# Kernel optimization log

Measured on AMD Instinct MI355X. Metric: run time of the kernel, lower is better.

Reference implementation:

```python
import jax, jax.numpy as jnp
import numpy as np

D = 1024
H = 16
HD = D // H
T = 2048
B = 2
EPS = 1e-6


def rmsnorm(x, w):
    xf = x.astype(jnp.float32)
    n = xf * jax.lax.rsqrt(jnp.mean(xf * xf, axis=-1, keepdims=True) + EPS)
    return n.astype(x.dtype) * w


def setup_inputs() -> dict:
    key = jax.random.key(0)
    ks = jax.random.split(key, 12)
    s_in = 1.0 / np.sqrt(D)
    s_h = 1.0 / np.sqrt(HD * H)
    s_ff = 1.0 / np.sqrt(4 * D)
    return {
        "x": jax.random.normal(ks[0], (B, T, D), jnp.float32),
        "wq": jax.random.normal(ks[1], (H, D, HD), jnp.float32) * s_in,
        "wk": jax.random.normal(ks[2], (H, D, HD), jnp.float32) * s_in,
        "wv": jax.random.normal(ks[3], (H, D, HD), jnp.float32) * s_in,
        "w_proj": jax.random.normal(ks[4], (D, D), jnp.float32) * s_h,
        "b_proj": jax.random.normal(ks[5], (D,), jnp.float32) * 0.01,
        "w1": jax.random.normal(ks[6], (D, 8 * D), jnp.float32) * s_in,
        "b1": jax.random.normal(ks[7], (8 * D,), jnp.float32) * 0.01,
        "w2": jax.random.normal(ks[8], (4 * D, D), jnp.float32) * s_ff,
        "b2": jax.random.normal(ks[9], (D,), jnp.float32) * 0.01,
        "g1": jnp.ones((D,), jnp.float32),
        "g2": jnp.ones((D,), jnp.float32),
    }


def reference(x, wq, wk, wv, w_proj, b_proj, w1, b1, w2, b2, g1, g2):
    # --- attention sub-block ---
    xn = rmsnorm(x, g1)
    q = jnp.einsum("btd,hde->bhte", xn, wq)  # [B,H,T,HD]
    k = jnp.einsum("btd,hde->bhte", xn, wk)
    v = jnp.einsum("btd,hde->bhte", xn, wv)
    scores = jnp.einsum("bhte,bhse->bhts", q, k) * (HD ** -0.5)
    causal = jnp.tril(jnp.ones((T, T), bool))
    scores = jnp.where(causal, scores, -jnp.inf)
    attn = jax.nn.softmax(scores, axis=-1)
    o = jnp.einsum("bhts,bhse->bhte", attn, v)  # [B,H,T,HD]
    o = o.transpose(0, 2, 1, 3).reshape(B, T, H * HD)  # concat heads
    x = x + o @ w_proj + b_proj
    # --- GLU FFN sub-block ---
    xn2 = rmsnorm(x, g2)
    h = xn2 @ w1 + b1  # [B,T,8D]
    a, b = jnp.split(h, 2, axis=-1)
    glu = a * jax.nn.sigmoid(b)  # [B,T,4D]
    x = x + glu @ w2 + b2
    return x
```

## Files before the change

### kernel.cpp

```cpp
#include <hip/hip_runtime.h>


typedef __attribute__((ext_vector_type(4))) float f32x4;
typedef __attribute__((ext_vector_type(8))) short short8;

typedef __attribute__((address_space(1))) const void gvoid;
typedef __attribute__((address_space(3))) void lvoid;

static __device__ __forceinline__ void gl_lds16(const void* g, void* l) {
  __builtin_amdgcn_global_load_lds((gvoid*)g, (lvoid*)l, 16, 0, 0);
}

static __device__ __forceinline__ unsigned short f2bf(float f) {
  union { float f; unsigned u; } v; v.f = f;
  unsigned r = v.u + 0x7fffu + ((v.u >> 16) & 1u);
  return (unsigned short)(r >> 16);
}
static __device__ __forceinline__ float to_f32(float v) { return v; }
static __device__ __forceinline__ float to_f32(unsigned short v) {
  union { unsigned u; float f; } x; x.u = ((unsigned)v) << 16; return x.f;
}

static __device__ __forceinline__ f32x4 mfma16(short8 a, short8 b, f32x4 c) {
  return __builtin_amdgcn_mfma_f32_16x16x32_bf16(a, b, c, 0, 0, 0);
}

__global__ __launch_bounds__(256) void prep_all(
    const float* __restrict__ wq, const float* __restrict__ wk,
    const float* __restrict__ wv, const float* __restrict__ wproj,
    const float* __restrict__ w1, const float* __restrict__ w2,
    unsigned short* __restrict__ wt_qkv, unsigned short* __restrict__ wpt,
    unsigned short* __restrict__ w1t, unsigned short* __restrict__ w2t,
    const float* __restrict__ x, const float* __restrict__ g1,
    unsigned short* __restrict__ xn)
{
  __shared__ float tile[64][65];
  const int bid = blockIdx.x;
  if (bid >= 4096) {
    int row = bid - 4096;
    int t = threadIdx.x;
    float4 v = ((const float4*)(x + (long)row * 1024))[t];
    float ss = v.x * v.x + v.y * v.y + v.z * v.z + v.w * v.w;
#pragma unroll
    for (int ofs = 32; ofs; ofs >>= 1) ss += __shfl_down(ss, ofs);
    float* red = &tile[0][0];
    if ((t & 63) == 0) red[t >> 6] = ss;
    __syncthreads();
    float sc = rsqrtf((red[0] + red[1] + red[2] + red[3]) * (1.0f / 1024.0f) + 1e-6f);
    float4 gv = ((const float4*)g1)[t];
    ushort4 o4;
    o4.x = f2bf(v.x * sc * gv.x); o4.y = f2bf(v.y * sc * gv.y);
    o4.z = f2bf(v.z * sc * gv.z); o4.w = f2bf(v.w * sc * gv.w);
    ((ushort4*)(xn + (long)row * 1024))[t] = o4;
    return;
  }
  const float* in;
  unsigned short* out;
  int r0, c0, in_ld, out_ld;
  if (bid < 768) {
    int z = bid >> 4, y = bid & 15;
    int head = z & 15, src = z >> 4;
    in = (src == 0 ? wq : src == 1 ? wk : wv) + (long)head * 1024 * 64;
    out = wt_qkv + ((long)src * 1024 + head * 64) * 1024;
    r0 = y * 64; c0 = 0; in_ld = 64; out_ld = 1024;
  } else if (bid < 1024) {
    int f = bid - 768;
    in = wproj; out = wpt;
    c0 = (f & 15) * 64; r0 = (f >> 4) * 64; in_ld = 1024; out_ld = 1024;
  } else if (bid < 3072) {
    int f = bid - 1024;
    in = w1; out = w1t;
    c0 = (f & 127) * 64; r0 = (f >> 7) * 64; in_ld = 8192; out_ld = 1024;
  } else {
    int f = bid - 3072;
    in = w2; out = w2t;
    c0 = (f & 15) * 64; r0 = (f >> 4) * 64; in_ld = 1024; out_ld = 4096;
  }
  int tx = threadIdx.x & 63, ty = threadIdx.x >> 6;
#pragma unroll
  for (int i = ty; i < 64; i += 4)
    tile[i][tx] = in[(long)(r0 + i) * in_ld + (c0 + tx)];
  __syncthreads();
#pragma unroll
  for (int i = ty; i < 64; i += 4)
    out[(long)(c0 + i) * out_ld + (r0 + tx)] = f2bf(tile[tx][i]);
}

__global__ __launch_bounds__(256) void rmsnorm_k(
    const float* __restrict__ x, const float* __restrict__ g,
    unsigned short* __restrict__ out)
{
  int row = blockIdx.x;
  int t = threadIdx.x;
  float4 v = ((const float4*)(x + (long)row * 1024))[t];
  float ss = v.x * v.x + v.y * v.y + v.z * v.z + v.w * v.w;
#pragma unroll
  for (int ofs = 32; ofs; ofs >>= 1) ss += __shfl_down(ss, ofs);
  __shared__ float red[4];
  if ((t & 63) == 0) red[t >> 6] = ss;
  __syncthreads();
  float sc = rsqrtf((red[0] + red[1] + red[2] + red[3]) * (1.0f / 1024.0f) + 1e-6f);
  float4 gv = ((const float4*)g)[t];
  ushort4 o4;
  o4.x = f2bf(v.x * sc * gv.x); o4.y = f2bf(v.y * sc * gv.y);
  o4.z = f2bf(v.z * sc * gv.z); o4.w = f2bf(v.w * sc * gv.w);
  ((ushort4*)(out + (long)row * 1024))[t] = o4;
}

template <int EPI, int BM, int BK, int WM_, int WN_, bool GLUB>
__global__ __launch_bounds__(256, 2) void gemm_bt(
    const unsigned short* __restrict__ A, const unsigned short* __restrict__ Bt,
    unsigned short* __restrict__ outb, float* __restrict__ outf,
    const float* __restrict__ res, const float* __restrict__ bias,
    unsigned short* __restrict__ vtout,
    int K, int lda, int ldbt, int ldout)
{
  constexpr int FM = BM / (16 * WM_);
  constexpr int FN = 128 / (16 * WN_);
  constexpr int KK = BK / 32;
  constexpr int UR = BK / 8;
  constexpr int ARn = BM * UR / 256;
  constexpr int BRn = 128 * UR / 256;
  constexpr int SPAN = 16 * FN;
  constexpr int HALF = SPAN / 2;
  __shared__ alignas(16) unsigned short Asm_[BM * BK];
  __shared__ alignas(16) unsigned short Bsm_[128 * BK];
  const int tid = threadIdx.x, lane = tid & 63, wave = tid >> 6;
  const int lr = lane & 15, lg = lane >> 4;
  const int wr = wave / WN_, wc = wave % WN_;
  const int m0 = blockIdx.y * BM;

  f32x4 acc[FM][FN];
#pragma unroll
  for (int mi = 0; mi < FM; mi++)
#pragma unroll
    for (int ni = 0; ni < FN; ni++) acc[mi][ni] = f32x4{0.f, 0.f, 0.f, 0.f};

  int rr_[BRn], ru_[BRn];
  long brow[BRn];
#pragma unroll
  for (int i = 0; i < BRn; i++) {
    int U = tid + 256 * i;
    int r = U / UR, u = U % UR;
    rr_[i] = r;
    ru_[i] = ((u & ~7) | ((u ^ r) & 7)) * 8;
    if (GLUB) {
      int w = r / SPAN, o = r % SPAN;
      brow[i] = (long)((o >= HALF) ? 4096 : 0) + blockIdx.x * 64 +
                w * HALF + (o % HALF);
    } else {
      brow[i] = (long)blockIdx.x * 128 + r;
    }
  }

  for (int k0 = 0; k0 < K; k0 += BK) {
#pragma unroll
    for (int i = 0; i < BRn; i++) {
      if (i < ARn)
        gl_lds16(A + (long)(m0 + rr_[i]) * lda + k0 + ru_[i],
                 (char*)Asm_ + (tid + 256 * i) * 16);
      gl_lds16(Bt + brow[i] * ldbt + k0 + ru_[i],
               (char*)Bsm_ + (tid + 256 * i) * 16);
    }
    __syncthreads();

    short8 af[FM][KK], bfr[FN][KK];
#pragma unroll
    for (int mi = 0; mi < FM; mi++) {
      int row = wr * 16 * FM + mi * 16 + lr;
#pragma unroll
      for (int kk = 0; kk < KK; kk++) {
        int u = kk * 4 + lg;
        int off = row * (2 * BK) + ((u & ~7) | ((u ^ (row & 7)) & 7)) * 16;
        af[mi][kk] = *(const short8*)((const char*)Asm_ + off);
      }
    }
#pragma unroll
    for (int ni = 0; ni < FN; ni++) {
      int row = wc * 16 * FN + ni * 16 + lr;
#pragma unroll
      for (int kk = 0; kk < KK; kk++) {
        int u = kk * 4 + lg;
        int off = row * (2 * BK) + ((u & ~7) | ((u ^ (row & 7)) & 7)) * 16;
        bfr[ni][kk] = *(const short8*)((const char*)Bsm_ + off);
      }
    }
#pragma unroll
    for (int kk = 0; kk < KK; kk++)
#pragma unroll
      for (int mi = 0; mi < FM; mi++)
#pragma unroll
        for (int ni = 0; ni < FN; ni++)
          acc[mi][ni] = mfma16(af[mi][kk], bfr[ni][kk], acc[mi][ni]);
    __syncthreads();
  }

  const int rb = m0 + wr * 16 * FM + 4 * lg;
  if constexpr (EPI == 0) {
#pragma unroll
    for (int mi = 0; mi < FM; mi++)
#pragma unroll
      for (int ni = 0; ni < FN; ni++) {
        int col = blockIdx.x * 128 + wc * 16 * FN + ni * 16 + lr;
#pragma unroll
        for (int r = 0; r < 4; r++)
          outb[(long)(rb + mi * 16 + r) * ldout + col] = f2bf(acc[mi][ni][r]);
      }
  } else if constexpr (EPI == 1) {
#pragma unroll
    for (int mi = 0; mi < FM; mi++)
#pragma unroll
      for (int ni = 0; ni < FN; ni++) {
        int col = blockIdx.x * 128 + wc * 16 * FN + ni * 16 + lr;
        float bv = bias[col];
#pragma unroll
        for (int r = 0; r < 4; r++) {
          long idx = (long)(rb + mi * 16 + r) * ldout + col;
          outf[idx] = acc[mi][ni][r] + res[idx] + bv;
        }
      }
  } else if constexpr (EPI == 2) {
#pragma unroll
    for (int mi = 0; mi < FM; mi++)
#pragma unroll
      for (int ni = 0; ni < FN / 2; ni++) {
        int col = blockIdx.x * 64 + wc * HALF + ni * 16 + lr;
        float ba = bias[col], bb2 = bias[4096 + col];
#pragma unroll
        for (int r = 0; r < 4; r++) {
          float a = acc[mi][ni][r] + ba;
          float b = acc[mi][ni + FN / 2][r] + bb2;
          float s = 1.0f / (1.0f + __expf(-b));
          outb[(long)(rb + mi * 16 + r) * ldout + col] = f2bf(a * s);
        }
      }
  } else {
#pragma unroll
    for (int mi = 0; mi < FM; mi++)
#pragma unroll
      for (int ni = 0; ni < FN; ni++) {
        int col = blockIdx.x * 128 + wc * 16 * FN + ni * 16 + lr;
        int row0 = rb + mi * 16;
        if (col < 2048) {
#pragma unroll
          for (int r = 0; r < 4; r++)
            outb[(long)(row0 + r) * ldout + col] = f2bf(acc[mi][ni][r]);
        } else {
          int c2 = col - 2048;
          int h = c2 >> 6, d = c2 & 63;
          int b = row0 >> 11, t = row0 & 2047;
          ushort4 o4;
          o4.x = f2bf(acc[mi][ni][0]); o4.y = f2bf(acc[mi][ni][1]);
          o4.z = f2bf(acc[mi][ni][2]); o4.w = f2bf(acc[mi][ni][3]);
          *(ushort4*)(vtout + ((long)((b << 4) | h) * 64 + d) * 2048 + t) = o4;
        }
      }
  }
}

__global__ __launch_bounds__(256, 2) void attn_k(
    const unsigned short* __restrict__ qkv, const unsigned short* __restrict__ vt,
    unsigned short* __restrict__ o)
{
  __shared__ alignas(16) unsigned short Ksm[2 * 128 * 64];
  __shared__ alignas(16) unsigned short Vsm[2 * 64 * 128];
  __shared__ alignas(16) unsigned short Psm[4][16 * 128];
  const int tid = threadIdx.x, lane = tid & 63, wave = tid >> 6;
  const int lr = lane & 15, lg = lane >> 4;
  const int bh = blockIdx.y, b = bh >> 4, h = bh & 15;
  const int ia = blockIdx.x;
  const int tA0 = ia * 64, tB0 = (31 - ia) * 64;
  const int nchA = (ia + 2) >> 1, nchB = (33 - ia) >> 1;
  const float NEGINF = -__builtin_inff();

  short8 qfA[2], qfB[2];
  {
    const unsigned short* qp =
        qkv + (long)(b * 2048 + tA0 + wave * 16 + lr) * 3072 + h * 64 + lg * 8;
    qfA[0] = *(const short8*)qp;  qfA[1] = *(const short8*)(qp + 32);
    qp = qkv + (long)(b * 2048 + tB0 + wave * 16 + lr) * 3072 + h * 64 + lg * 8;
    qfB[0] = *(const short8*)qp;  qfB[1] = *(const short8*)(qp + 32);
  }
  f32x4 oA[4], oB[4];
#pragma unroll
  for (int n = 0; n < 4; n++) { oA[n] = f32x4{0,0,0,0}; oB[n] = f32x4{0,0,0,0}; }
  float mA = NEGINF, lA = 0.f, mB = NEGINF, lB = 0.f;

  const long kbase = (long)(b * 2048) * 3072 + 1024 + h * 64;
  const long vbase = (long)bh * 64 * 2048;

  auto stage = [&](int buf, int c) {
    const int s0 = c * 128;
#pragma unroll
    for (int i = 0; i < 4; i++) {
      int U = tid + 256 * i;
      int kr = U >> 3, ku = (U ^ kr) & 7;
      gl_lds16(qkv + kbase + (long)(s0 + kr) * 3072 + ku * 8,
               (char*)Ksm + (buf * 1024 + wave * 64 + 256 * i) * 16);
      int vr = U >> 4, vu = (U & 8) | ((U ^ vr) & 7);
      gl_lds16(vt + vbase + (long)vr * 2048 + s0 + vu * 8,
               (char*)Vsm + (buf * 1024 + wave * 64 + 256 * i) * 16);
    }
  };

  char* pb = (char*)&Psm[wave][0];

  auto qk = [&](const short8* qf, f32x4* s, const char* kb) {
#pragma unroll
    for (int n = 0; n < 8; n++) s[n] = f32x4{0.f, 0.f, 0.f, 0.f};
#pragma unroll
    for (int n = 0; n < 8; n++) {
      int row = n * 16 + lr;
#pragma unroll
      for (int kk = 0; kk < 2; kk++) {
        int off = row * 128 + (((kk * 4 + lg) ^ row) & 7) * 16;
        short8 kf = *(const short8*)(kb + off);
        s[n] = mfma16(kf, qf[kk], s[n]);
      }
    }
  };

  auto smpv = [&](f32x4* s, f32x4* o_acc, float& m, float& l,
                  const char* vb, int s0, int qg, bool diag) {
#pragma unroll
    for (int n = 0; n < 8; n++)
#pragma unroll
      for (int r = 0; r < 4; r++) {
        float v = s[n][r] * 0.125f;
        if (diag && (s0 + n * 16 + 4 * lg + r > qg)) v = NEGINF;
        s[n][r] = v;
      }
    float t[8];
#pragma unroll
    for (int n = 0; n < 8; n++)
      t[n] = fmaxf(fmaxf(s[n][0], s[n][1]), fmaxf(s[n][2], s[n][3]));
    float mx = fmaxf(fmaxf(fmaxf(t[0], t[1]), fmaxf(t[2], t[3])),
                     fmaxf(fmaxf(t[4], t[5]), fmaxf(t[6], t[7])));
    mx = fmaxf(mx, __shfl_xor(mx, 16));
    mx = fmaxf(mx, __shfl_xor(mx, 32));
    if (!__all(mx <= m + 8.0f)) {
      float mn = fmaxf(m, mx);
      float alpha = __expf(m - mn);
      m = mn;
      l *= alpha;
#pragma unroll
      for (int r = 0; r < 4; r++) {
        float ar = __shfl(alpha, 4 * lg + r);
#pragma unroll
        for (int n = 0; n < 4; n++) o_acc[n][r] *= ar;
      }
    }
    float sum = 0.f;
#pragma unroll
    for (int n = 0; n < 8; n++)
#pragma unroll
      for (int r = 0; r < 4; r++) {
        float p = __expf(s[n][r] - m);
        s[n][r] = p;
        sum += p;
      }
    sum += __shfl_xor(sum, 16);
    sum += __shfl_xor(sum, 32);
    l += sum;
#pragma unroll
    for (int n = 0; n < 8; n++) {
      unsigned lo = (unsigned)f2bf(s[n][0]) | ((unsigned)f2bf(s[n][1]) << 16);
      unsigned hi = (unsigned)f2bf(s[n][2]) | ((unsigned)f2bf(s[n][3]) << 16);
      int u = 2 * n + (lg >> 1);
      int su = (u & 8) | ((u ^ lr) & 7);
      *(uint2*)(pb + lr * 256 + su * 16 + 8 * (lg & 1)) = uint2{lo, hi};
    }
    asm volatile("s_waitcnt lgkmcnt(0)" ::: "memory");
    __builtin_amdgcn_sched_barrier(0);
    short8 pa[4];
#pragma unroll
    for (int ks = 0; ks < 4; ks++) {
      int u = 4 * ks + lg;
      int su = (u & 8) | ((u ^ lr) & 7);
      pa[ks] = *(const short8*)(pb + lr * 256 + su * 16);
    }
    __builtin_amdgcn_s_setprio(1);
#pragma unroll
    for (int n = 0; n < 4; n++) {
      int row = n * 16 + lr;
#pragma unroll
      for (int ks = 0; ks < 4; ks++) {
        int u = 4 * ks + lg;
        int su = (u & 8) | ((u ^ row) & 7);
        short8 vf = *(const short8*)(vb + row * 256 + su * 16);
        o_acc[n] = mfma16(pa[ks], vf, o_acc[n]);
      }
    }
    __builtin_amdgcn_s_setprio(0);
  };

  stage(0, 0);
  __syncthreads();

  const int qgA = tA0 + wave * 16 + lr, qgB = tB0 + wave * 16 + lr;
  for (int c = 0; c < nchB; c++) {
    if (c + 1 < nchB) stage((c + 1) & 1, c + 1);
    const char* kb = (const char*)Ksm + (c & 1) * 16384;
    const char* vb = (const char*)Vsm + (c & 1) * 16384;
    const int s0 = c * 128;
    const bool doA = (c < nchA);
    f32x4 sA[8], sB[8];
    __builtin_amdgcn_s_setprio(1);
    if (doA) qk(qfA, sA, kb);
    qk(qfB, sB, kb);
    __builtin_amdgcn_s_setprio(0);
    if (doA) smpv(sA, oA, mA, lA, vb, s0, qgA, c == nchA - 1);
    smpv(sB, oB, mB, lB, vb, s0, qgB, c == nchB - 1);
    __syncthreads();
  }

  auto finish = [&](const f32x4* o_acc, float l, int t0) {
#pragma unroll
    for (int r = 0; r < 4; r++) {
      float inv = 1.0f / __shfl(l, 4 * lg + r);
      int trow = t0 + wave * 16 + 4 * lg + r;
#pragma unroll
      for (int n = 0; n < 4; n++)
        o[(long)(b * 2048 + trow) * 1024 + h * 64 + n * 16 + lr] =
            f2bf(o_acc[n][r] * inv);
    }
  };
  finish(oA, lA, tA0);
  finish(oB, lB, tB0);
}

extern "C" void kernel_launch(void* const* d_in, const int* in_sizes, int n_in,
                              void* d_out, int out_size, void* d_ws, size_t ws_size,
                              hipStream_t stream) {
  const float* x     = (const float*)d_in[0];
  const float* wq    = (const float*)d_in[1];
  const float* wk    = (const float*)d_in[2];
  const float* wv    = (const float*)d_in[3];
  const float* wproj = (const float*)d_in[4];
  const float* bproj = (const float*)d_in[5];
  const float* w1    = (const float*)d_in[6];
  const float* b1    = (const float*)d_in[7];
  const float* w2    = (const float*)d_in[8];
  const float* b2    = (const float*)d_in[9];
  const float* g1    = (const float*)d_in[10];
  const float* g2    = (const float*)d_in[11];
  (void)in_sizes; (void)n_in; (void)out_size; (void)ws_size;

  char* ws = (char*)d_ws;
  unsigned short* wt_qkv = (unsigned short*)(ws);
  unsigned short* wpt    = (unsigned short*)(ws + (6ul << 20));
  unsigned short* w1t    = (unsigned short*)(ws + (8ul << 20));
  unsigned short* w2t    = (unsigned short*)(ws + (24ul << 20));
  unsigned short* xn     = (unsigned short*)(ws + (32ul << 20));
  unsigned short* qkv    = (unsigned short*)(ws + (40ul << 20));
  unsigned short* vt     = (unsigned short*)(ws + (64ul << 20));
  unsigned short* glu    = (unsigned short*)(ws + (40ul << 20));
  unsigned short* obuf   = (unsigned short*)(ws + (72ul << 20));
  float*          x1     = (float*)(ws + (80ul << 20));
  float* outf = (float*)d_out;

  prep_all<<<8192, 256, 0, stream>>>(wq, wk, wv, wproj, w1, w2,
                                     wt_qkv, wpt, w1t, w2t, x, g1, xn);

  gemm_bt<3, 128, 64, 2, 2, false><<<dim3(24, 32), 256, 0, stream>>>(
      xn, wt_qkv, qkv, nullptr, nullptr, nullptr, vt, 1024, 1024, 1024, 3072);

  attn_k<<<dim3(16, 32), 256, 0, stream>>>(qkv, vt, obuf);

  gemm_bt<1, 64, 128, 2, 2, false><<<dim3(8, 64), 256, 0, stream>>>(
      obuf, wpt, nullptr, x1, x, bproj, nullptr, 1024, 1024, 1024, 1024);

  rmsnorm_k<<<4096, 256, 0, stream>>>(x1, g2, xn);

  gemm_bt<2, 128, 64, 2, 2, true><<<dim3(64, 32), 256, 0, stream>>>(
      xn, w1t, glu, nullptr, nullptr, b1, nullptr, 1024, 1024, 1024, 4096);

  gemm_bt<1, 64, 128, 2, 2, false><<<dim3(8, 64), 256, 0, stream>>>(
      glu, w2t, nullptr, outf, x1, b2, nullptr, 4096, 4096, 4096, 1024);
}
```

Measured before the change: 260.4 us.

## Replace GLU GEMM with 256x256 eight-wave double-buffered pipelined kernel

The FFN up-projection with fused GLU epilogue moves from the generic 128x128 gemm_bt to a dedicated 512-thread kernel. Each block computes a 256x256 tile (128 gate/value column pairs), with LDS double buffering, staged async global-to-LDS loads interleaved with MFMA quadrants, and setprio around the MFMA bursts. The goal is more data reuse per block and overlap of memory loads with compute in the largest GEMM. In exchange it needs more LDS and registers (one block per CU) and relies on hand-placed waitcnt and barrier sequencing that must stay correct.

```diff
diff --git a/kernel.cpp b/kernel.cpp
--- a/kernel.cpp
+++ b/kernel.cpp
@@ -107,7 +107,7 @@
   ((ushort4*)(out + (long)row * 1024))[t] = o4;
 }
 
-template <int EPI, int BM, int BK, int WM_, int WN_, bool GLUB>
+template <int EPI, int BM, int BK, int WM_, int WN_>
 __global__ __launch_bounds__(256, 2) void gemm_bt(
     const unsigned short* __restrict__ A, const unsigned short* __restrict__ Bt,
     unsigned short* __restrict__ outb, float* __restrict__ outf,
@@ -121,8 +121,6 @@
   constexpr int UR = BK / 8;
   constexpr int ARn = BM * UR / 256;
   constexpr int BRn = 128 * UR / 256;
-  constexpr int SPAN = 16 * FN;
-  constexpr int HALF = SPAN / 2;
   __shared__ alignas(16) unsigned short Asm_[BM * BK];
   __shared__ alignas(16) unsigned short Bsm_[128 * BK];
   const int tid = threadIdx.x, lane = tid & 63, wave = tid >> 6;
@@ -144,13 +142,7 @@
     int r = U / UR, u = U % UR;
     rr_[i] = r;
     ru_[i] = ((u & ~7) | ((u ^ r) & 7)) * 8;
-    if (GLUB) {
-      int w = r / SPAN, o = r % SPAN;
-      brow[i] = (long)((o >= HALF) ? 4096 : 0) + blockIdx.x * 64 +
-                w * HALF + (o % HALF);
-    } else {
-      brow[i] = (long)blockIdx.x * 128 + r;
-    }
+    brow[i] = (long)blockIdx.x * 128 + r;
   }
 
   for (int k0 = 0; k0 < K; k0 += BK) {
@@ -217,21 +209,6 @@
         for (int r = 0; r < 4; r++) {
           long idx = (long)(rb + mi * 16 + r) * ldout + col;
           outf[idx] = acc[mi][ni][r] + res[idx] + bv;
-        }
-      }
-  } else if constexpr (EPI == 2) {
-#pragma unroll
-    for (int mi = 0; mi < FM; mi++)
-#pragma unroll
-      for (int ni = 0; ni < FN / 2; ni++) {
-        int col = blockIdx.x * 64 + wc * HALF + ni * 16 + lr;
-        float ba = bias[col], bb2 = bias[4096 + col];
-#pragma unroll
-        for (int r = 0; r < 4; r++) {
-          float a = acc[mi][ni][r] + ba;
-          float b = acc[mi][ni + FN / 2][r] + bb2;
-          float s = 1.0f / (1.0f + __expf(-b));
-          outb[(long)(rb + mi * 16 + r) * ldout + col] = f2bf(a * s);
         }
       }
   } else {
@@ -256,6 +233,136 @@
         }
       }
   }
+}
+
+__global__ __launch_bounds__(512, 1) void gemm8_glu(
+    const unsigned short* __restrict__ A, const unsigned short* __restrict__ Bt,
+    unsigned short* __restrict__ outb, const float* __restrict__ bias,
+    int K, int lda, int ldbt, int ldout)
+{
+  __shared__ alignas(16) unsigned short Asm_[2][2][128 * 64];
+  __shared__ alignas(16) unsigned short Bsm_[2][2][128 * 64];
+  const int tid = threadIdx.x, lane = tid & 63, wave = tid >> 6;
+  const int lr = lane & 15, lg = lane >> 4;
+  const int wr = wave >> 2, wc = wave & 3;
+  const int m0 = blockIdx.y * 256;
+  const int bx = blockIdx.x;
+
+  f32x4 acc[8][4];
+#pragma unroll
+  for (int mi = 0; mi < 8; mi++)
+#pragma unroll
+    for (int ni = 0; ni < 4; ni++) acc[mi][ni] = f32x4{0.f, 0.f, 0.f, 0.f};
+
+  auto stageA = [&](int buf, int h, int kt) {
+#pragma unroll
+    for (int i = 0; i < 2; i++) {
+      int U = tid + 512 * i;
+      int r = U >> 3, s = (U ^ r) & 7;
+      gl_lds16(A + (long)(m0 + h * 128 + r) * lda + kt * 64 + s * 8,
+               (char*)&Asm_[buf][h][0] + U * 16);
+    }
+  };
+  auto stageB = [&](int buf, int h, int kt) {
+#pragma unroll
+    for (int i = 0; i < 2; i++) {
+      int U = tid + 512 * i;
+      int r = U >> 3, s = (U ^ r) & 7;
+      int row = h * 128 + r;
+      int w = row >> 6, o = row & 63;
+      long br = (o < 32) ? (long)(bx * 128 + w * 32 + o)
+                         : (long)4096 + bx * 128 + w * 32 + (o - 32);
+      gl_lds16(Bt + br * ldbt + kt * 64 + s * 8,
+               (char*)&Bsm_[buf][h][0] + U * 16);
+    }
+  };
+  auto lda8 = [&](int buf, int mi, int kk) -> short8 {
+    int rl = mi * 16 + lr;
+    int u = kk * 4 + lg;
+    return *(const short8*)((const char*)&Asm_[buf][wr][0] + rl * 128 +
+                            ((u ^ (rl & 7)) * 16));
+  };
+  auto ldb8 = [&](int buf, int ni, int kk) -> short8 {
+    int row = wc * 64 + ni * 16 + lr;
+    int h = row >> 7, rl = row & 127;
+    int u = kk * 4 + lg;
+    return *(const short8*)((const char*)&Bsm_[buf][h][0] + rl * 128 +
+                            ((u ^ (rl & 7)) * 16));
+  };
+
+  short8 af[4][2], bf0[2][2], bf1[2][2];
+#define QUAD(BF, MI0, NI0)                                                   \
+  do {                                                                       \
+    __builtin_amdgcn_s_setprio(1);                                           \
+    _Pragma("unroll") for (int kk_ = 0; kk_ < 2; kk_++)                      \
+    _Pragma("unroll") for (int mi_ = 0; mi_ < 4; mi_++)                      \
+    _Pragma("unroll") for (int ni_ = 0; ni_ < 2; ni_++)                      \
+      acc[(MI0) + mi_][(NI0) + ni_] =                                        \
+          mfma16(af[mi_][kk_], BF[ni_][kk_], acc[(MI0) + mi_][(NI0) + ni_]); \
+    __builtin_amdgcn_s_setprio(0);                                           \
+  } while (0)
+
+  stageB(0, 0, 0); stageB(0, 1, 0); stageA(0, 0, 0); stageA(0, 1, 0);
+  stageB(1, 0, 1); stageB(1, 1, 1); stageA(1, 0, 1);
+  asm volatile("s_waitcnt vmcnt(6)" ::: "memory");
+  __builtin_amdgcn_s_barrier();
+
+  const int NT = K / 64;
+  for (int u = 0; u < NT; ++u) {
+    const int buf = u & 1;
+#pragma unroll
+    for (int mi = 0; mi < 4; mi++)
+#pragma unroll
+      for (int kk = 0; kk < 2; kk++) af[mi][kk] = lda8(buf, mi, kk);
+#pragma unroll
+    for (int ni = 0; ni < 2; ni++)
+#pragma unroll
+      for (int kk = 0; kk < 2; kk++) bf0[ni][kk] = ldb8(buf, ni, kk);
+    if (u + 1 < NT) stageA(buf ^ 1, 1, u + 1);
+    __builtin_amdgcn_s_barrier();
+    asm volatile("s_waitcnt lgkmcnt(0)" ::: "memory");
+    QUAD(bf0, 0, 0);
+    __builtin_amdgcn_s_barrier();
+#pragma unroll
+    for (int ni = 0; ni < 2; ni++)
+#pragma unroll
+      for (int kk = 0; kk < 2; kk++) bf1[ni][kk] = ldb8(buf, ni + 2, kk);
+    __builtin_amdgcn_s_barrier();
+    asm volatile("s_waitcnt lgkmcnt(0)" ::: "memory");
+    QUAD(bf1, 0, 2);
+    __builtin_amdgcn_s_barrier();
+#pragma unroll
+    for (int mi = 0; mi < 4; mi++)
+#pragma unroll
+      for (int kk = 0; kk < 2; kk++) af[mi][kk] = lda8(buf, mi + 4, kk);
+    if (u + 2 < NT) stageB(buf, 0, u + 2);
+    __builtin_amdgcn_s_barrier();
+    asm volatile("s_waitcnt lgkmcnt(0)" ::: "memory");
+    QUAD(bf1, 4, 2);
+    __builtin_amdgcn_s_barrier();
+    if (u + 2 < NT) { stageB(buf, 1, u + 2); stageA(buf, 0, u + 2); }
+    QUAD(bf0, 4, 0);
+    if (u == NT - 2)     asm volatile("s_waitcnt vmcnt(0)" ::: "memory");
+    else if (u < NT - 2) asm volatile("s_waitcnt vmcnt(6)" ::: "memory");
+    __builtin_amdgcn_s_barrier();
+  }
+#undef QUAD
+
+#pragma unroll
+  for (int mi = 0; mi < 8; mi++)
+#pragma unroll
+    for (int ni = 0; ni < 2; ni++) {
+      int col = bx * 128 + wc * 32 + ni * 16 + lr;
+      float ba = bias[col], bb = bias[4096 + col];
+#pragma unroll
+      for (int r = 0; r < 4; r++) {
+        int row = m0 + wr * 128 + mi * 16 + 4 * lg + r;
+        float a = acc[mi][ni][r] + ba;
+        float b = acc[mi][ni + 2][r] + bb;
+        float s = 1.0f / (1.0f + __expf(-b));
+        outb[(long)row * ldout + col] = f2bf(a * s);
+      }
+    }
 }
 
 __global__ __launch_bounds__(256, 2) void attn_k(
@@ -462,19 +569,19 @@
   prep_all<<<8192, 256, 0, stream>>>(wq, wk, wv, wproj, w1, w2,
                                      wt_qkv, wpt, w1t, w2t, x, g1, xn);
 
-  gemm_bt<3, 128, 64, 2, 2, false><<<dim3(24, 32), 256, 0, stream>>>(
+  gemm_bt<3, 128, 64, 2, 2><<<dim3(24, 32), 256, 0, stream>>>(
       xn, wt_qkv, qkv, nullptr, nullptr, nullptr, vt, 1024, 1024, 1024, 3072);
 
   attn_k<<<dim3(16, 32), 256, 0, stream>>>(qkv, vt, obuf);
 
-  gemm_bt<1, 64, 128, 2, 2, false><<<dim3(8, 64), 256, 0, stream>>>(
+  gemm_bt<1, 64, 128, 2, 2><<<dim3(8, 64), 256, 0, stream>>>(
       obuf, wpt, nullptr, x1, x, bproj, nullptr, 1024, 1024, 1024, 1024);
 
   rmsnorm_k<<<4096, 256, 0, stream>>>(x1, g2, xn);
 
-  gemm_bt<2, 128, 64, 2, 2, true><<<dim3(64, 32), 256, 0, stream>>>(
-      xn, w1t, glu, nullptr, nullptr, b1, nullptr, 1024, 1024, 1024, 4096);
-
-  gemm_bt<1, 64, 128, 2, 2, false><<<dim3(8, 64), 256, 0, stream>>>(
+  gemm8_glu<<<dim3(32, 16), 512, 0, stream>>>(
+      xn, w1t, glu, b1, 1024, 1024, 1024, 4096);
+
+  gemm_bt<1, 64, 128, 2, 2><<<dim3(8, 64), 256, 0, stream>>>(
       glu, w2t, nullptr, outf, x1, b2, nullptr, 4096, 4096, 4096, 1024);
 }
```

New measurement: 268.3 us. +3.1%, slower.
